# Kernel tuning notes

Hardware: AMD Instinct MI355X
Metric: run time of the kernel (lower is better)

The kernel has to match this reference:

```python
import jax, jax.numpy as jnp
import numpy as np

INPUT_SIZE = 1
HIDDEN = 64
B, T = 1024, 1024


def setup_inputs() -> dict:
    key = jax.random.key(0)
    ks = jax.random.split(key, 16)
    s = 1.0 / np.sqrt(HIDDEN)  # PyTorch LSTM init scale
    def u(k, shape):
        return jax.random.uniform(k, shape, jnp.float32, -s, s)
    x = jax.random.normal(ks[0], (B, T, INPUT_SIZE), jnp.float32)
    return {
        "x": x,
        # layer 0 (input_size -> hidden), gate order i,f,g,o stacked along 4H
        "W_ih0": u(ks[1], (4 * HIDDEN, INPUT_SIZE)),
        "W_hh0": u(ks[2], (4 * HIDDEN, HIDDEN)),
        "b_ih0": u(ks[3], (4 * HIDDEN,)),
        "b_hh0": u(ks[4], (4 * HIDDEN,)),
        # layer 1 (hidden -> hidden)
        "W_ih1": u(ks[5], (4 * HIDDEN, HIDDEN)),
        "W_hh1": u(ks[6], (4 * HIDDEN, HIDDEN)),
        "b_ih1": u(ks[7], (4 * HIDDEN,)),
        "b_hh1": u(ks[8], (4 * HIDDEN,)),
        # FC head: Linear(64,32) -> ReLU -> Linear(32,1)
        "fc1_w": u(ks[9], (HIDDEN // 2, HIDDEN)),
        "fc1_b": u(ks[10], (HIDDEN // 2,)),
        "fc2_w": u(ks[11], (1, HIDDEN // 2)),
        "fc2_b": u(ks[12], (1,)),
    }


def _lstm_layer(x_seq, W_ih, W_hh, b_ih, b_hh):
    """One LSTM layer over [B, T, D_in] -> hidden sequence [B, T, H]."""
    Bsz = x_seq.shape[0]
    H = W_hh.shape[1]
    # precompute input projection for all timesteps: [B, T, 4H]
    xW = jnp.einsum("btd,gd->btg", x_seq, W_ih) + b_ih + b_hh
    Whh_T = W_hh.T  # [H, 4H]

    def step(carry, xw_t):
        h, c = carry
        gates = xw_t + h @ Whh_T  # [B, 4H]
        i, f, g, o = jnp.split(gates, 4, axis=-1)
        i = jax.nn.sigmoid(i)
        f = jax.nn.sigmoid(f)
        g = jnp.tanh(g)
        o = jax.nn.sigmoid(o)
        c = f * c + i * g
        h = o * jnp.tanh(c)
        return (h, c), h

    h0 = jnp.zeros((Bsz, H), x_seq.dtype)
    (_, _), hs = jax.lax.scan(step, (h0, h0), jnp.swapaxes(xW, 0, 1))
    return jnp.swapaxes(hs, 0, 1)  # [B, T, H]


def reference(x, W_ih0, W_hh0, b_ih0, b_hh0, W_ih1, W_hh1, b_ih1, b_hh1,
              fc1_w, fc1_b, fc2_w, fc2_b):
    # 2-layer LSTM (inference: inter-layer dropout is identity)
    h1 = _lstm_layer(x, W_ih0, W_hh0, b_ih0, b_hh0)
    h2 = _lstm_layer(h1, W_ih1, W_hh1, b_ih1, b_hh1)
    last = h2[:, -1, :]  # [B, H]
    z = jax.nn.relu(last @ fc1_w.T + fc1_b)
    out = z @ fc2_w.T + fc2_b  # [B, 1]
    return out.squeeze(-1)  # [B]
```

## Files before the change

kernel.cpp:

```cpp
#include <hip/hip_runtime.h>

#define HID  64
#define SEQT 1024
#define NB   4

typedef _Float16 h8 __attribute__((ext_vector_type(8)));
typedef float    f4 __attribute__((ext_vector_type(4)));
typedef float    v2f __attribute__((ext_vector_type(2)));

__device__ __forceinline__ float rcpf(float x){ return __builtin_amdgcn_rcpf(x); }
__device__ __forceinline__ float sigm(float x){ return rcpf(1.0f + __expf(-x)); }
__device__ __forceinline__ float tanh_fast(float x){
    return 1.0f - 2.0f * rcpf(__expf(2.0f * x) + 1.0f);
}
__device__ __forceinline__ v2f pkfma(v2f a, v2f b, v2f c){
    return __builtin_elementwise_fma(a, b, c);
}

#define MFMA16(A,B,C) __builtin_amdgcn_mfma_f32_16x16x32_f16((A),(B),(C),0,0,0)

__device__ __forceinline__ h8 cvt8(const float* __restrict__ p) {
    float4 u = *(const float4*)p;
    float4 v = *(const float4*)(p + 4);
    h8 r;
    r[0] = (_Float16)u.x; r[1] = (_Float16)u.y;
    r[2] = (_Float16)u.z; r[3] = (_Float16)u.w;
    r[4] = (_Float16)v.x; r[5] = (_Float16)v.y;
    r[6] = (_Float16)v.z; r[7] = (_Float16)v.w;
    return r;
}

__global__ __launch_bounds__(1024, 4)
void lstm2_v16(const float* __restrict__ x,
               const float* __restrict__ W_ih0, const float* __restrict__ W_hh0,
               const float* __restrict__ b_ih0, const float* __restrict__ b_hh0,
               const float* __restrict__ W_ih1, const float* __restrict__ W_hh1,
               const float* __restrict__ b_ih1, const float* __restrict__ b_hh1,
               const float* __restrict__ fc1_w, const float* __restrict__ fc1_b,
               const float* __restrict__ fc2_w, const float* __restrict__ fc2_b,
               float* __restrict__ out, int nblk)
{
    const int blk = blockIdx.x;
    if (blk >= nblk) return;
    const int tid = threadIdx.x;
    const int w   = tid >> 6;
    const int l   = tid & 63;
    const int r16 = l & 15;
    const int g4  = l >> 4;
    const int cc  = r16 & 3;
    const int cb  = w & 3;
    const int B0  = blk * NB;

    __shared__ __align__(16) _Float16 h1f[2][NB][80];
    __shared__ __align__(16) _Float16 h2f16[2][NB][80];
    __shared__ __align__(16) float G0[NB][260];
    __shared__ __align__(16) float G1[NB][260];
    __shared__ __align__(16) float h2fin[NB][64];

    h8 a0[2];
    h8 a1[4];
    {
        const int row = 16 * w + r16;
        #pragma unroll
        for (int ks = 0; ks < 2; ++ks) {
            a0[ks]     = cvt8(W_hh0 + row * HID + ks * 32 + g4 * 8);
            a1[ks]     = cvt8(W_ih1 + row * HID + ks * 32 + g4 * 8);
            a1[2 + ks] = cvt8(W_hh1 + row * HID + ks * 32 + g4 * 8);
        }
    }

    const float* bip = (w < 4) ? b_ih0 : b_ih1;
    const float* bhp = (w < 4) ? b_hh0 : b_hh1;
    v2f biasA, biasB, wihA, wihB;
    biasA.x = bip[l]       + bhp[l];
    biasA.y = bip[l + 64]  + bhp[l + 64];
    biasB.x = bip[l + 128] + bhp[l + 128];
    biasB.y = bip[l + 192] + bhp[l + 192];
    if (w < 4) {
        wihA.x = W_ih0[l];       wihA.y = W_ih0[l + 64];
        wihB.x = W_ih0[l + 128]; wihB.y = W_ih0[l + 192];
    } else {
        wihA = (v2f){0.f, 0.f};  wihB = (v2f){0.f, 0.f};
    }

    if (tid < 320) {
        ((int*)h1f)[tid] = 0; ((int*)h2f16)[tid] = 0;
    }
    const size_t xbase = (size_t)(B0 + cb) * SEQT;
    float xc = 0.0f, xcn = 0.0f;
    if (w < 4) xc = x[xbase + l];
    float cst = 0.0f;
    __syncthreads();

    const f4 z4 = {0.f, 0.f, 0.f, 0.f};
    const bool meC0 = (w < 4);
    const bool meC1 = (w >= 4 && w < 8);

    auto step = [&](int t_, int P,
                    bool L0A, bool G1A, bool C0A, bool C1A, bool FIN) {
        const int RB1 = P ^ 1;

        if (meC0 && ((t_ & 63) == 0) && (t_ + 64 < SEQT))
            xcn = x[xbase + t_ + 64 + l];

        h8 b1h0, b1h1;
        if (L0A || G1A) {
            b1h0 = *(const h8*)&h1f[RB1][cc][g4 * 8];
            b1h1 = *(const h8*)&h1f[RB1][cc][32 + g4 * 8];
        }
        v2f gA1, gB1;
        if (C1A && meC1) {
            gA1 = (v2f){G1[cb][l],       G1[cb][l + 64]};
            gB1 = (v2f){G1[cb][l + 128], G1[cb][l + 192]};
        }
        __builtin_amdgcn_s_setprio(1);
        if (L0A) {
            f4 e = MFMA16(a0[0], b1h0, z4);
            e = MFMA16(a0[1], b1h1, e);
            if (r16 < NB)
                *(f4*)&G0[r16][16 * w + 4 * g4] = e;
        }
        __builtin_amdgcn_s_setprio(0);
        if (C1A && meC1) {
            v2f pA = gA1 + biasA;
            v2f pB = gB1 + biasB;
            float iv = sigm(pA.x), fv = sigm(pA.y);
            float gv = tanh_fast(pB.x), ov = sigm(pB.y);
            cst = fmaf(fv, cst, iv * gv);
            float hv = ov * tanh_fast(cst);
            _Float16 hh = (_Float16)hv;
            h2f16[P][cb][l] = hh;
            if (FIN) h2fin[cb][l] = (float)hh;
        }
        __syncthreads();

        v2f gA0, gB0;
        if (C0A && meC0) {
            gA0 = (v2f){G0[w][l],       G0[w][l + 64]};
            gB0 = (v2f){G0[w][l + 128], G0[w][l + 192]};
        }
        __builtin_amdgcn_s_setprio(1);
        if (G1A) {
            h8 b2h0 = *(const h8*)&h2f16[P][cc][g4 * 8];
            h8 b2h1 = *(const h8*)&h2f16[P][cc][32 + g4 * 8];
            f4 p = MFMA16(a1[0], b1h0, z4);
            p = MFMA16(a1[1], b1h1, p);
            p = MFMA16(a1[2], b2h0, p);
            p = MFMA16(a1[3], b2h1, p);
            if (r16 < NB)
                *(f4*)&G1[r16][16 * w + 4 * g4] = p;
        }
        __builtin_amdgcn_s_setprio(0);
        if (C0A && meC0) {
            const float xt = __shfl(xc, t_ & 63);
            v2f xt2 = {xt, xt};
            v2f pA = gA0 + pkfma(xt2, wihA, biasA);
            v2f pB = gB0 + pkfma(xt2, wihB, biasB);
            float iv = sigm(pA.x), fv = sigm(pA.y);
            float gv = tanh_fast(pB.x), ov = sigm(pB.y);
            cst = fmaf(fv, cst, iv * gv);
            float hv = ov * tanh_fast(cst);
            h1f[P][w][l] = (_Float16)hv;
        }
        if ((t_ & 63) == 63) xc = xcn;
        __syncthreads();
    };

    step(        0,    0, true,  false, true,  false, false);
    step(        1,    1, true,  true,  true,  false, false);
    #pragma unroll 1
    for (int t = 2; t < SEQT; t += 2) {
        step(t,      0, true,  true,  true,  true,  false);
        step(t + 1,  1, true,  true,  true,  true,  false);
    }
    step(     SEQT,    0, false, true,  false, true,  false);
    step( SEQT + 1,    1, false, false, false, true,  true );

    if (w < 4) {
        float z = 0.0f;
        if (l < 32) {
            float acc = fc1_b[l];
            const f4* hvp = (const f4*)h2fin[w];
            const f4* wvp = (const f4*)(fc1_w + l * HID);
            #pragma unroll
            for (int q = 0; q < 16; ++q) {
                f4 hq = hvp[q], wk = wvp[q];
                acc = fmaf(hq[0], wk[0], acc); acc = fmaf(hq[1], wk[1], acc);
                acc = fmaf(hq[2], wk[2], acc); acc = fmaf(hq[3], wk[3], acc);
            }
            z = fmaxf(acc, 0.0f) * fc2_w[l];
        }
        #pragma unroll
        for (int off = 32; off > 0; off >>= 1) z += __shfl_xor(z, off);
        if (l == 0) out[B0 + w] = z + fc2_b[0];
    }
}

extern "C" void kernel_launch(void* const* d_in, const int* in_sizes, int n_in,
                              void* d_out, int out_size, void* d_ws, size_t ws_size,
                              hipStream_t stream) {
    const float* x     = (const float*)d_in[0];
    const float* W_ih0 = (const float*)d_in[1];
    const float* W_hh0 = (const float*)d_in[2];
    const float* b_ih0 = (const float*)d_in[3];
    const float* b_hh0 = (const float*)d_in[4];
    const float* W_ih1 = (const float*)d_in[5];
    const float* W_hh1 = (const float*)d_in[6];
    const float* b_ih1 = (const float*)d_in[7];
    const float* b_hh1 = (const float*)d_in[8];
    const float* fc1_w = (const float*)d_in[9];
    const float* fc1_b = (const float*)d_in[10];
    const float* fc2_w = (const float*)d_in[11];
    const float* fc2_b = (const float*)d_in[12];
    float* out = (float*)d_out;

    const int batch = in_sizes[0] / SEQT;
    const int nblk  = batch / NB;
    dim3 grid(nblk), block(1024);
    hipLaunchKernelGGL(lstm2_v16, grid, block, 0, stream,
                       x, W_ih0, W_hh0, b_ih0, b_hh0,
                       W_ih1, W_hh1, b_ih1, b_hh1,
                       fc1_w, fc1_b, fc2_w, fc2_b, out, nblk);
}
```

Measured before the change: 590.2 us.

## Halve batch per block and give each wave two MFMA row tiles

Each block now handles 2 batch rows with 512 threads (8 waves) instead of 4 rows with 1024 threads. Each wave computes two 16-row gate tiles, with interleaved independent MFMA chains, rather than one. The goal is a shorter, cheaper per-step barrier and twice as many blocks (512) to fill the CUs, while MFMA tiles stay 16 columns wide and now carry only 2 useful batch columns. The trade-off is more MFMA work per useful output and more registers per wave.

Result: slower. 894.7 us (+51.6%).

```diff
diff --git a/kernel.cpp b/kernel.cpp
--- a/kernel.cpp
+++ b/kernel.cpp
@@ -2,7 +2,7 @@
 
 #define HID  64
 #define SEQT 1024
-#define NB   4
+#define NB   2
 
 typedef _Float16 h8 __attribute__((ext_vector_type(8)));
 typedef float    f4 __attribute__((ext_vector_type(4)));
@@ -30,8 +30,8 @@
     return r;
 }
 
-__global__ __launch_bounds__(1024, 4)
-void lstm2_v16(const float* __restrict__ x,
+__global__ __launch_bounds__(512, 4)
+void lstm2_v17(const float* __restrict__ x,
                const float* __restrict__ W_ih0, const float* __restrict__ W_hh0,
                const float* __restrict__ b_ih0, const float* __restrict__ b_hh0,
                const float* __restrict__ W_ih1, const float* __restrict__ W_hh1,
@@ -47,8 +47,7 @@
     const int l   = tid & 63;
     const int r16 = l & 15;
     const int g4  = l >> 4;
-    const int cc  = r16 & 3;
-    const int cb  = w & 3;
+    const int cc  = r16 & 1;
     const int B0  = blk * NB;
 
     __shared__ __align__(16) _Float16 h1f[2][NB][80];
@@ -57,44 +56,46 @@
     __shared__ __align__(16) float G1[NB][260];
     __shared__ __align__(16) float h2fin[NB][64];
 
-    h8 a0[2];
-    h8 a1[4];
-    {
-        const int row = 16 * w + r16;
+    h8 a0[2][2];
+    h8 a1[2][4];
+    #pragma unroll
+    for (int tt = 0; tt < 2; ++tt) {
+        const int row = 32 * w + 16 * tt + r16;
         #pragma unroll
         for (int ks = 0; ks < 2; ++ks) {
-            a0[ks]     = cvt8(W_hh0 + row * HID + ks * 32 + g4 * 8);
-            a1[ks]     = cvt8(W_ih1 + row * HID + ks * 32 + g4 * 8);
-            a1[2 + ks] = cvt8(W_hh1 + row * HID + ks * 32 + g4 * 8);
-        }
-    }
-
-    const float* bip = (w < 4) ? b_ih0 : b_ih1;
-    const float* bhp = (w < 4) ? b_hh0 : b_hh1;
+            a0[tt][ks]     = cvt8(W_hh0 + row * HID + ks * 32 + g4 * 8);
+            a1[tt][ks]     = cvt8(W_ih1 + row * HID + ks * 32 + g4 * 8);
+            a1[tt][2 + ks] = cvt8(W_hh1 + row * HID + ks * 32 + g4 * 8);
+        }
+    }
+
+    const bool meC0 = (w < 2);
+    const bool meC1 = (w >= 2 && w < 4);
+    const int  cb   = meC0 ? w : (w - 2);
+    const float* bip = meC0 ? b_ih0 : b_ih1;
+    const float* bhp = meC0 ? b_hh0 : b_hh1;
     v2f biasA, biasB, wihA, wihB;
     biasA.x = bip[l]       + bhp[l];
     biasA.y = bip[l + 64]  + bhp[l + 64];
     biasB.x = bip[l + 128] + bhp[l + 128];
     biasB.y = bip[l + 192] + bhp[l + 192];
-    if (w < 4) {
+    if (meC0) {
         wihA.x = W_ih0[l];       wihA.y = W_ih0[l + 64];
         wihB.x = W_ih0[l + 128]; wihB.y = W_ih0[l + 192];
     } else {
         wihA = (v2f){0.f, 0.f};  wihB = (v2f){0.f, 0.f};
     }
 
-    if (tid < 320) {
+    if (tid < 160) {
         ((int*)h1f)[tid] = 0; ((int*)h2f16)[tid] = 0;
     }
     const size_t xbase = (size_t)(B0 + cb) * SEQT;
     float xc = 0.0f, xcn = 0.0f;
-    if (w < 4) xc = x[xbase + l];
+    if (meC0) xc = x[xbase + l];
     float cst = 0.0f;
     __syncthreads();
 
     const f4 z4 = {0.f, 0.f, 0.f, 0.f};
-    const bool meC0 = (w < 4);
-    const bool meC1 = (w >= 4 && w < 8);
 
     auto step = [&](int t_, int P,
                     bool L0A, bool G1A, bool C0A, bool C1A, bool FIN) {
@@ -115,10 +116,14 @@
         }
         __builtin_amdgcn_s_setprio(1);
         if (L0A) {
-            f4 e = MFMA16(a0[0], b1h0, z4);
-            e = MFMA16(a0[1], b1h1, e);
-            if (r16 < NB)
-                *(f4*)&G0[r16][16 * w + 4 * g4] = e;
+            f4 e0 = MFMA16(a0[0][0], b1h0, z4);
+            f4 e1 = MFMA16(a0[1][0], b1h0, z4);
+            e0 = MFMA16(a0[0][1], b1h1, e0);
+            e1 = MFMA16(a0[1][1], b1h1, e1);
+            if (r16 < NB) {
+                *(f4*)&G0[r16][32 * w + 4 * g4]      = e0;
+                *(f4*)&G0[r16][32 * w + 16 + 4 * g4] = e1;
+            }
         }
         __builtin_amdgcn_s_setprio(0);
         if (C1A && meC1) {
@@ -136,19 +141,25 @@
 
         v2f gA0, gB0;
         if (C0A && meC0) {
-            gA0 = (v2f){G0[w][l],       G0[w][l + 64]};
-            gB0 = (v2f){G0[w][l + 128], G0[w][l + 192]};
+            gA0 = (v2f){G0[cb][l],       G0[cb][l + 64]};
+            gB0 = (v2f){G0[cb][l + 128], G0[cb][l + 192]};
         }
         __builtin_amdgcn_s_setprio(1);
         if (G1A) {
             h8 b2h0 = *(const h8*)&h2f16[P][cc][g4 * 8];
             h8 b2h1 = *(const h8*)&h2f16[P][cc][32 + g4 * 8];
-            f4 p = MFMA16(a1[0], b1h0, z4);
-            p = MFMA16(a1[1], b1h1, p);
-            p = MFMA16(a1[2], b2h0, p);
-            p = MFMA16(a1[3], b2h1, p);
-            if (r16 < NB)
-                *(f4*)&G1[r16][16 * w + 4 * g4] = p;
+            f4 p0 = MFMA16(a1[0][0], b1h0, z4);
+            f4 p1 = MFMA16(a1[1][0], b1h0, z4);
+            p0 = MFMA16(a1[0][1], b1h1, p0);
+            p1 = MFMA16(a1[1][1], b1h1, p1);
+            p0 = MFMA16(a1[0][2], b2h0, p0);
+            p1 = MFMA16(a1[1][2], b2h0, p1);
+            p0 = MFMA16(a1[0][3], b2h1, p0);
+            p1 = MFMA16(a1[1][3], b2h1, p1);
+            if (r16 < NB) {
+                *(f4*)&G1[r16][32 * w + 4 * g4]      = p0;
+                *(f4*)&G1[r16][32 * w + 16 + 4 * g4] = p1;
+            }
         }
         __builtin_amdgcn_s_setprio(0);
         if (C0A && meC0) {
@@ -160,7 +171,7 @@
             float gv = tanh_fast(pB.x), ov = sigm(pB.y);
             cst = fmaf(fv, cst, iv * gv);
             float hv = ov * tanh_fast(cst);
-            h1f[P][w][l] = (_Float16)hv;
+            h1f[P][cb][l] = (_Float16)hv;
         }
         if ((t_ & 63) == 63) xc = xcn;
         __syncthreads();
@@ -176,7 +187,7 @@
     step(     SEQT,    0, false, true,  false, true,  false);
     step( SEQT + 1,    1, false, false, false, true,  true );
 
-    if (w < 4) {
+    if (w < 2) {
         float z = 0.0f;
         if (l < 32) {
             float acc = fc1_b[l];
@@ -216,8 +227,8 @@
 
     const int batch = in_sizes[0] / SEQT;
     const int nblk  = batch / NB;
-    dim3 grid(nblk), block(1024);
-    hipLaunchKernelGGL(lstm2_v16, grid, block, 0, stream,
+    dim3 grid(nblk), block(512);
+    hipLaunchKernelGGL(lstm2_v17, grid, block, 0, stream,
                        x, W_ih0, W_hh0, b_ih0, b_hh0,
                        W_ih1, W_hh1, b_ih1, b_hh1,
                        fc1_w, fc1_b, fc2_w, fc2_b, out, nblk);
```
